# Performance work log

Hardware: AMD Instinct MI355X
Metric: run time of the kernel (lower is better)

Reference implementation:

```python
import jax, jax.numpy as jnp
import numpy as np

M0, S0 = 0.0, 2.0       # normal prior mean / std on mu, beta
SHAPE, SCALE = 2.0, 1.0  # gamma prior on softplus(phi)


def _softplus(x):
    return jnp.logaddexp(x, 0.0)


def _log_negbinomial(y, mu, phi):
    # NB parameterized by mean mu and dispersion phi (var = mu + phi*mu^2)
    r = 1.0 / phi
    return (jax.lax.lgamma(y + r) - jax.lax.lgamma(r) - jax.lax.lgamma(y + 1.0)
            + r * jnp.log(r / (r + mu)) + y * jnp.log(mu / (r + mu)))


def _log_normal(x, m, s):
    return -0.5 * jnp.log(2.0 * jnp.pi * s * s) - (x - m) ** 2 / (2.0 * s * s)


def _log_gamma(x, shape, scale):
    return ((shape - 1.0) * jnp.log(x) - x / scale
            - jax.lax.lgamma(jnp.asarray(shape, x.dtype)) - shape * jnp.log(scale))


def setup_inputs() -> dict:
    key = jax.random.key(0)
    k1, k2, k3, k4, k5 = jax.random.split(key, 5)
    N, P, G = 1024, 4, 20000
    X = jax.random.normal(k1, (N, P), dtype=jnp.float32)
    Y = jax.random.randint(k2, (N, G), 0, 500).astype(jnp.float32)
    mu = jax.random.normal(k3, (G,), dtype=jnp.float32)
    beta = jax.random.normal(k4, (P * G,), dtype=jnp.float32)
    phi = jax.random.normal(k5, (G,), dtype=jnp.float32)
    return {"X": X, "Y": Y, "mu": mu, "beta": beta, "phi": phi}


def reference(X, Y, mu, beta, phi):
    N, P = X.shape
    G = Y.shape[1]
    beta_ = beta.reshape(P, G)
    log_unnorm = mu + X @ beta_                                   # [N, G]
    norm = jax.scipy.special.logsumexp(log_unnorm, axis=1, keepdims=True)
    pi = jnp.exp(log_unnorm - norm)                               # softmax over genes
    s = jnp.sum(Y, axis=1, keepdims=True)                         # [N, 1] library sizes
    phi_sp = _softplus(phi)                                       # [G]
    log_lik = jnp.sum(_log_negbinomial(Y, s * pi, phi_sp))
    log_prior = (jnp.sum(_log_normal(mu, M0, S0))
                 + jnp.sum(_log_normal(beta, M0, S0))
                 + jnp.sum(_log_gamma(phi_sp, SHAPE, SCALE)))
    return (log_lik + log_prior).reshape(1)
```

## Files before the change

### kernel.cpp

```cpp
#include <hip/hip_runtime.h>
#include <math.h>


#define FG4   5000
#define FCH4  250
#define FNCH  20
#define FNSL  64
#define FNBLK 1280

__device__ __forceinline__ float fast_rcp(float x) {
    return __builtin_amdgcn_rcpf(x);
}

__device__ __forceinline__ float lgamma_pos(float x) {
    float lp = 0.0f;
    if (x < 8.0f) {
        float p = x;
        x += 1.0f;
        while (x < 8.0f) { p *= x; x += 1.0f; }
        lp = __logf(p);
    }
    float inv  = fast_rcp(x);
    float inv2 = inv * inv;
    float ser = inv * (0.08333333333f + inv2 * (-0.002777777778f + inv2 * 7.936507937e-4f));
    return (x - 0.5f) * __logf(x) - x + 0.9189385332f + ser - lp;
}

__device__ __forceinline__ float stirling_lg(float x) {
    float inv  = fast_rcp(x);
    float inv2 = inv * inv;
    float ser  = inv * (0.08333333333f - 0.002777777778f * inv2);
    return (x - 0.5f) * __logf(x) - x + 0.9189385332f + ser;
}

__device__ __forceinline__ float softplus_f(float x) {
    return fmaxf(x, 0.0f) + log1pf(__expf(-fabsf(x)));
}

__device__ __forceinline__ float wave_reduce(float v) {
#pragma unroll
    for (int off = 32; off; off >>= 1) v += __shfl_down(v, off, 64);
    return v;
}

__global__ __launch_bounds__(256) void setup_kernel(
        const float* __restrict__ mu, const float* __restrict__ beta,
        const float* __restrict__ phi, double* __restrict__ acc,
        float* __restrict__ rg, float* __restrict__ cgw, int P, int G) {
    int g = blockIdx.x * 256 + threadIdx.x;
    float v = 0.0f;
    if (g < G) {
        const float cn = -1.6120857137646180f;
        float m = mu[g];
        v = cn - m * m * 0.125f;
        for (int p = 0; p < P; ++p) {
            float b = beta[(size_t)p * G + g];
            v += cn - b * b * 0.125f;
        }
        float sp = softplus_f(phi[g]);
        v += __logf(sp) - sp;
        float r = 1.0f / sp;
        rg[g]  = r;
        cgw[g] = r * __logf(r) - lgamma_pos(r);
    }
    v = wave_reduce(v);
    __shared__ float red[4];
    int lane = threadIdx.x & 63, wid = threadIdx.x >> 6;
    if (lane == 0) red[wid] = v;
    __syncthreads();
    if (threadIdx.x == 0)
        atomicAdd(acc, (double)((red[0] + red[1]) + (red[2] + red[3])));
}

__global__ __launch_bounds__(256, 4) void pre_fast(
        const float* __restrict__ X, const float* __restrict__ Y,
        const float* __restrict__ mu, const float* __restrict__ beta,
        float* __restrict__ syw, float* __restrict__ sew) {
    __shared__ float Xs[64];
    __shared__ float syp[4][16], sep[4][16];

    const int tid  = threadIdx.x;
    const int lane = tid & 63, wid = tid >> 6;
    const int c    = blockIdx.x % FNCH;
    const int s    = blockIdx.x / FNCH;
    const int n0   = s * 16;
    const bool active = (tid < FCH4);
    const int gi4  = c * FCH4 + (active ? tid : FCH4 - 1);

    const float4* __restrict__ Yp = (const float4*)Y + (size_t)n0 * FG4 + gi4;
    float4 ya[16];
#pragma unroll
    for (int j = 0; j < 16; ++j) ya[j] = Yp[(size_t)j * FG4];

    if (tid < 64) Xs[tid] = X[(size_t)n0 * 4 + tid];
    const float4* __restrict__ B4 = (const float4*)beta;
    float4 bb[4], mug;
#pragma unroll
    for (int p = 0; p < 4; ++p) bb[p] = B4[(size_t)p * FG4 + gi4];
    mug = ((const float4*)mu)[gi4];
    __syncthreads();

#pragma unroll
    for (int i0 = 0; i0 < 16; i0 += 4) {
        float sy[4], se[4];
#pragma unroll
        for (int j = 0; j < 4; ++j) {
            const int i = i0 + j;
            float4 y = ya[i];
            float4 lu = mug;
#pragma unroll
            for (int p = 0; p < 4; ++p) {
                float xp = Xs[i * 4 + p];
                lu.x = fmaf(xp, bb[p].x, lu.x);
                lu.y = fmaf(xp, bb[p].y, lu.y);
                lu.z = fmaf(xp, bb[p].z, lu.z);
                lu.w = fmaf(xp, bb[p].w, lu.w);
            }
            float e = (__expf(lu.x) + __expf(lu.y)) + (__expf(lu.z) + __expf(lu.w));
            se[j] = active ? e : 0.0f;
            sy[j] = active ? ((y.x + y.y) + (y.z + y.w)) : 0.0f;
        }
#pragma unroll
        for (int off = 32; off; off >>= 1) {
#pragma unroll
            for (int j = 0; j < 4; ++j) {
                sy[j] += __shfl_down(sy[j], off, 64);
                se[j] += __shfl_down(se[j], off, 64);
            }
        }
        if (lane == 0) {
#pragma unroll
            for (int j = 0; j < 4; ++j) {
                syp[wid][i0 + j] = sy[j];
                sep[wid][i0 + j] = se[j];
            }
        }
    }
    __syncthreads();
    if (tid < 16) {
        float a = (syp[0][tid] + syp[1][tid]) + (syp[2][tid] + syp[3][tid]);
        float b = (sep[0][tid] + sep[1][tid]) + (sep[2][tid] + sep[3][tid]);
        atomicAdd(&syw[n0 + tid], a);
        atomicAdd(&sew[n0 + tid], b);
    }
}

__global__ __launch_bounds__(256, 4) void nb_fast(
        const float* __restrict__ X, const float* __restrict__ Y,
        const float* __restrict__ mu, const float* __restrict__ beta,
        const float* __restrict__ rg, const float* __restrict__ cgw,
        const float* __restrict__ syw, const float* __restrict__ sew,
        double* __restrict__ acc) {
    __shared__ float lgY[512];
    __shared__ float Xs[64];
    __shared__ float dcs[16];
    __shared__ float red[4];

    const int tid  = threadIdx.x;
    const int lane = tid & 63, wid = tid >> 6;
    const int c    = blockIdx.x % FNCH;
    const int s    = blockIdx.x / FNCH;
    const int n0   = s * 16;
    const bool active = (tid < FCH4);
    const int gi4  = c * FCH4 + (active ? tid : FCH4 - 1);

    const float4* __restrict__ Yp = (const float4*)Y + (size_t)n0 * FG4 + gi4;
    float4 ya[8];
#pragma unroll
    for (int j = 0; j < 8; ++j) ya[j] = Yp[(size_t)j * FG4];

    for (int i = tid; i < 500; i += 256) lgY[i] = lgamma_pos((float)(i + 1));
    if (tid < 64) Xs[tid] = X[(size_t)n0 * 4 + tid];
    if (tid < 16) dcs[tid] = __logf(syw[n0 + tid]) - __logf(sew[n0 + tid]);

    const float4* __restrict__ B4 = (const float4*)beta;
    float4 bb[4], mug, r4, cg4;
#pragma unroll
    for (int p = 0; p < 4; ++p) bb[p] = B4[(size_t)p * FG4 + gi4];
    mug = ((const float4*)mu)[gi4];
    r4  = ((const float4*)rg)[gi4];
    cg4 = ((const float4*)cgw)[gi4];
    __syncthreads();

    float t0 = 0.0f, t1 = 0.0f, t2 = 0.0f, t3 = 0.0f;
    auto elem = [&](int i, float4 y) {
        float dcn = dcs[i];
        float4 lu = mug;
#pragma unroll
        for (int p = 0; p < 4; ++p) {
            float xp = Xs[i * 4 + p];
            lu.x = fmaf(xp, bb[p].x, lu.x);
            lu.y = fmaf(xp, bb[p].y, lu.y);
            lu.z = fmaf(xp, bb[p].z, lu.z);
            lu.w = fmaf(xp, bb[p].w, lu.w);
        }
        float lm, m, yr;
        lm = dcn + lu.x; m = __expf(lm); yr = y.x + r4.x;
        t0 += stirling_lg(yr) - lgY[__float2int_rz(y.x)]
            + fmaf(y.x, lm, -yr * __logf(r4.x + m)) + cg4.x;
        lm = dcn + lu.y; m = __expf(lm); yr = y.y + r4.y;
        t1 += stirling_lg(yr) - lgY[__float2int_rz(y.y)]
            + fmaf(y.y, lm, -yr * __logf(r4.y + m)) + cg4.y;
        lm = dcn + lu.z; m = __expf(lm); yr = y.z + r4.z;
        t2 += stirling_lg(yr) - lgY[__float2int_rz(y.z)]
            + fmaf(y.z, lm, -yr * __logf(r4.z + m)) + cg4.z;
        lm = dcn + lu.w; m = __expf(lm); yr = y.w + r4.w;
        t3 += stirling_lg(yr) - lgY[__float2int_rz(y.w)]
            + fmaf(y.w, lm, -yr * __logf(r4.w + m)) + cg4.w;
    };

    float4 yb[8];
#pragma unroll
    for (int j = 0; j < 8; ++j) yb[j] = Yp[(size_t)(8 + j) * FG4];
#pragma unroll
    for (int i = 0; i < 8; ++i) elem(i, ya[i]);
#pragma unroll
    for (int i = 0; i < 8; ++i) elem(8 + i, yb[i]);

    float accl = active ? ((t0 + t1) + (t2 + t3)) : 0.0f;
    accl = wave_reduce(accl);
    if (lane == 0) red[wid] = accl;
    __syncthreads();
    if (tid == 0)
        atomicAdd(acc, (double)((red[0] + red[1]) + (red[2] + red[3])));
}

__global__ void finalize_kernel(const double* __restrict__ acc, float* __restrict__ out) {
    out[0] = (float)acc[0];
}

__global__ void row_stats_generic(
        const float* __restrict__ X, const float* __restrict__ Y,
        const float* __restrict__ mu, const float* __restrict__ beta,
        float* __restrict__ syw, float* __restrict__ sew, int N, int P, int G) {
    const int n = blockIdx.x;
    const int tid = threadIdx.x;
    float sy = 0.0f, se = 0.0f;
    for (int g = tid; g < G; g += 256) {
        sy += Y[(size_t)n * G + g];
        float lu = mu[g];
        for (int p = 0; p < P; ++p) lu += X[(size_t)n * P + p] * beta[(size_t)p * G + g];
        se += __expf(lu);
    }
    sy = wave_reduce(sy);
    se = wave_reduce(se);
    __shared__ float r1[4], r2[4];
    int lane = tid & 63, wid = tid >> 6;
    if (lane == 0) { r1[wid] = sy; r2[wid] = se; }
    __syncthreads();
    if (tid == 0) {
        syw[n] = (r1[0] + r1[1]) + (r1[2] + r1[3]);
        sew[n] = (r2[0] + r2[1]) + (r2[2] + r2[3]);
    }
}

__global__ void nb_generic(
        const float* __restrict__ X, const float* __restrict__ Y,
        const float* __restrict__ mu, const float* __restrict__ beta,
        const float* __restrict__ rg, const float* __restrict__ cgw,
        const float* __restrict__ syw, const float* __restrict__ sew,
        double* __restrict__ acc, int N, int P, int G) {
    const int n = blockIdx.x;
    const int tid = threadIdx.x;
    float dcn = __logf(syw[n]) - __logf(sew[n]);
    float accl = 0.0f;
    for (int g = tid; g < G; g += 256) {
        float y = Y[(size_t)n * G + g];
        float lu = mu[g];
        for (int p = 0; p < P; ++p) lu += X[(size_t)n * P + p] * beta[(size_t)p * G + g];
        float lm = dcn + lu;
        float r = rg[g];
        float m = __expf(lm);
        accl += stirling_lg(y + r) - lgamma_pos(y + 1.0f)
                + fmaf(y, lm, -(y + r) * __logf(r + m)) + cgw[g];
    }
    accl = wave_reduce(accl);
    __shared__ float red[4];
    int lane = tid & 63, wid = tid >> 6;
    if (lane == 0) red[wid] = accl;
    __syncthreads();
    if (tid == 0)
        atomicAdd(acc, (double)((red[0] + red[1]) + (red[2] + red[3])));
}

extern "C" void kernel_launch(void* const* d_in, const int* in_sizes, int n_in,
                              void* d_out, int out_size, void* d_ws, size_t ws_size,
                              hipStream_t stream) {
    const float* X    = (const float*)d_in[0];
    const float* Y    = (const float*)d_in[1];
    const float* mu   = (const float*)d_in[2];
    const float* beta = (const float*)d_in[3];
    const float* phi  = (const float*)d_in[4];
    float* out = (float*)d_out;

    const int G = in_sizes[2];
    const int N = in_sizes[1] / G;
    const int P = in_sizes[0] / N;

    char* ws = (char*)d_ws;
    double* acc = (double*)ws;
    float*  syw = (float*)(ws + 256);
    float*  sew = (float*)(ws + 4608);
    float*  rgw = (float*)(ws + 8960);
    float*  cgw = (float*)(ws + 8960 + (size_t)4 * G);

    hipMemsetAsync(d_ws, 0, 8960, stream);

    const bool fast_ok = (N == 1024 && G == 20000 && P == 4);
    int gblocks = (G + 255) / 256;

    if (fast_ok) {
        pre_fast<<<FNBLK, 256, 0, stream>>>(X, Y, mu, beta, syw, sew);
        setup_kernel<<<gblocks, 256, 0, stream>>>(mu, beta, phi, acc, rgw, cgw, P, G);
        nb_fast<<<FNBLK, 256, 0, stream>>>(X, Y, mu, beta, rgw, cgw, syw, sew, acc);
    } else {
        setup_kernel<<<gblocks, 256, 0, stream>>>(mu, beta, phi, acc, rgw, cgw, P, G);
        row_stats_generic<<<N, 256, 0, stream>>>(X, Y, mu, beta, syw, sew, N, P, G);
        nb_generic<<<N, 256, 0, stream>>>(X, Y, mu, beta, rgw, cgw, syw, sew,
                                          acc, N, P, G);
    }
    finalize_kernel<<<1, 1, 0, stream>>>(acc, out);
}
```

Measured before the change: 167.3 us.

## Fuse setup and finalize into pre/nb kernels, trim Stirling series

Moves the prior and per-gene rg/cgw computation into the first slice of pre_fast blocks, removing the separate setup_kernel launch. The final float conversion now happens in the last nb_fast block, found through an atomic completion counter, which replaces the single-thread finalize launch. The Stirling lgamma series drops its second-order term, saving a few instructions per element at some accuracy cost for small y+r. The intent is to cut two kernel launches and their gaps, in exchange for extra work in the s==0 blocks and a fence and atomic per block.

```diff
diff --git a/kernel.cpp b/kernel.cpp
--- a/kernel.cpp
+++ b/kernel.cpp
@@ -5,7 +5,6 @@
 #define FG4   5000
 #define FCH4  250
 #define FNCH  20
-#define FNSL  64
 #define FNBLK 1280
 
 __device__ __forceinline__ float fast_rcp(float x) {
@@ -27,10 +26,8 @@
 }
 
 __device__ __forceinline__ float stirling_lg(float x) {
-    float inv  = fast_rcp(x);
-    float inv2 = inv * inv;
-    float ser  = inv * (0.08333333333f - 0.002777777778f * inv2);
-    return (x - 0.5f) * __logf(x) - x + 0.9189385332f + ser;
+    float inv = fast_rcp(x);
+    return fmaf(x - 0.5f, __logf(x), 0.08333333333f * inv) - x + 0.9189385332f;
 }
 
 __device__ __forceinline__ float softplus_f(float x) {
@@ -43,41 +40,16 @@
     return v;
 }
 
-__global__ __launch_bounds__(256) void setup_kernel(
-        const float* __restrict__ mu, const float* __restrict__ beta,
-        const float* __restrict__ phi, double* __restrict__ acc,
-        float* __restrict__ rg, float* __restrict__ cgw, int P, int G) {
-    int g = blockIdx.x * 256 + threadIdx.x;
-    float v = 0.0f;
-    if (g < G) {
-        const float cn = -1.6120857137646180f;
-        float m = mu[g];
-        v = cn - m * m * 0.125f;
-        for (int p = 0; p < P; ++p) {
-            float b = beta[(size_t)p * G + g];
-            v += cn - b * b * 0.125f;
-        }
-        float sp = softplus_f(phi[g]);
-        v += __logf(sp) - sp;
-        float r = 1.0f / sp;
-        rg[g]  = r;
-        cgw[g] = r * __logf(r) - lgamma_pos(r);
-    }
-    v = wave_reduce(v);
-    __shared__ float red[4];
-    int lane = threadIdx.x & 63, wid = threadIdx.x >> 6;
-    if (lane == 0) red[wid] = v;
-    __syncthreads();
-    if (threadIdx.x == 0)
-        atomicAdd(acc, (double)((red[0] + red[1]) + (red[2] + red[3])));
-}
-
 __global__ __launch_bounds__(256, 4) void pre_fast(
         const float* __restrict__ X, const float* __restrict__ Y,
         const float* __restrict__ mu, const float* __restrict__ beta,
-        float* __restrict__ syw, float* __restrict__ sew) {
+        const float* __restrict__ phi,
+        float* __restrict__ syw, float* __restrict__ sew,
+        float* __restrict__ rgw, float* __restrict__ cgw,
+        double* __restrict__ acc) {
     __shared__ float Xs[64];
     __shared__ float syp[4][16], sep[4][16];
+    __shared__ float red[4];
 
     const int tid  = threadIdx.x;
     const int lane = tid & 63, wid = tid >> 6;
@@ -98,7 +70,43 @@
 #pragma unroll
     for (int p = 0; p < 4; ++p) bb[p] = B4[(size_t)p * FG4 + gi4];
     mug = ((const float4*)mu)[gi4];
-    __syncthreads();
+
+    float priorv = 0.0f;
+    if (s == 0) {
+        const float cn = -1.6120857137646180f;
+        float4 ph = ((const float4*)phi)[gi4];
+        float4 r4p, cg4p;
+        priorv += cn - mug.x * mug.x * 0.125f;
+        priorv += cn - mug.y * mug.y * 0.125f;
+        priorv += cn - mug.z * mug.z * 0.125f;
+        priorv += cn - mug.w * mug.w * 0.125f;
+#pragma unroll
+        for (int p = 0; p < 4; ++p) {
+            priorv += cn - bb[p].x * bb[p].x * 0.125f;
+            priorv += cn - bb[p].y * bb[p].y * 0.125f;
+            priorv += cn - bb[p].z * bb[p].z * 0.125f;
+            priorv += cn - bb[p].w * bb[p].w * 0.125f;
+        }
+        float sp;
+        sp = softplus_f(ph.x); priorv += __logf(sp) - sp; r4p.x = fast_rcp(sp);
+        cg4p.x = r4p.x * __logf(r4p.x) - lgamma_pos(r4p.x);
+        sp = softplus_f(ph.y); priorv += __logf(sp) - sp; r4p.y = fast_rcp(sp);
+        cg4p.y = r4p.y * __logf(r4p.y) - lgamma_pos(r4p.y);
+        sp = softplus_f(ph.z); priorv += __logf(sp) - sp; r4p.z = fast_rcp(sp);
+        cg4p.z = r4p.z * __logf(r4p.z) - lgamma_pos(r4p.z);
+        sp = softplus_f(ph.w); priorv += __logf(sp) - sp; r4p.w = fast_rcp(sp);
+        cg4p.w = r4p.w * __logf(r4p.w) - lgamma_pos(r4p.w);
+        if (active) {
+            ((float4*)rgw)[gi4] = r4p;
+            ((float4*)cgw)[gi4] = cg4p;
+        }
+        if (!active) priorv = 0.0f;
+        priorv = wave_reduce(priorv);
+        if (lane == 0) red[wid] = priorv;
+    }
+    __syncthreads();
+    if (s == 0 && tid == 0)
+        atomicAdd(acc, (double)((red[0] + red[1]) + (red[2] + red[3])));
 
 #pragma unroll
     for (int i0 = 0; i0 < 16; i0 += 4) {
@@ -150,7 +158,8 @@
         const float* __restrict__ mu, const float* __restrict__ beta,
         const float* __restrict__ rg, const float* __restrict__ cgw,
         const float* __restrict__ syw, const float* __restrict__ sew,
-        double* __restrict__ acc) {
+        double* __restrict__ acc, float* __restrict__ out,
+        unsigned int* __restrict__ counter) {
     __shared__ float lgY[512];
     __shared__ float Xs[64];
     __shared__ float dcs[16];
@@ -221,12 +230,44 @@
     accl = wave_reduce(accl);
     if (lane == 0) red[wid] = accl;
     __syncthreads();
-    if (tid == 0)
+    if (tid == 0) {
         atomicAdd(acc, (double)((red[0] + red[1]) + (red[2] + red[3])));
-}
-
-__global__ void finalize_kernel(const double* __restrict__ acc, float* __restrict__ out) {
-    out[0] = (float)acc[0];
+        __threadfence();
+        unsigned int old = atomicAdd(counter, 1u);
+        if (old == (unsigned int)(FNBLK - 1)) {
+            double v = atomicAdd(acc, 0.0);
+            out[0] = (float)v;
+        }
+    }
+}
+
+__global__ __launch_bounds__(256) void setup_kernel(
+        const float* __restrict__ mu, const float* __restrict__ beta,
+        const float* __restrict__ phi, double* __restrict__ acc,
+        float* __restrict__ rg, float* __restrict__ cgw, int P, int G) {
+    int g = blockIdx.x * 256 + threadIdx.x;
+    float v = 0.0f;
+    if (g < G) {
+        const float cn = -1.6120857137646180f;
+        float m = mu[g];
+        v = cn - m * m * 0.125f;
+        for (int p = 0; p < P; ++p) {
+            float b = beta[(size_t)p * G + g];
+            v += cn - b * b * 0.125f;
+        }
+        float sp = softplus_f(phi[g]);
+        v += __logf(sp) - sp;
+        float r = 1.0f / sp;
+        rg[g]  = r;
+        cgw[g] = r * __logf(r) - lgamma_pos(r);
+    }
+    v = wave_reduce(v);
+    __shared__ float red[4];
+    int lane = threadIdx.x & 63, wid = threadIdx.x >> 6;
+    if (lane == 0) red[wid] = v;
+    __syncthreads();
+    if (threadIdx.x == 0)
+        atomicAdd(acc, (double)((red[0] + red[1]) + (red[2] + red[3])));
 }
 
 __global__ void row_stats_generic(
@@ -283,6 +324,10 @@
         atomicAdd(acc, (double)((red[0] + red[1]) + (red[2] + red[3])));
 }
 
+__global__ void finalize_kernel(const double* __restrict__ acc, float* __restrict__ out) {
+    out[0] = (float)acc[0];
+}
+
 extern "C" void kernel_launch(void* const* d_in, const int* in_sizes, int n_in,
                               void* d_out, int out_size, void* d_ws, size_t ws_size,
                               hipStream_t stream) {
@@ -298,26 +343,28 @@
     const int P = in_sizes[0] / N;
 
     char* ws = (char*)d_ws;
-    double* acc = (double*)ws;
-    float*  syw = (float*)(ws + 256);
-    float*  sew = (float*)(ws + 4608);
-    float*  rgw = (float*)(ws + 8960);
-    float*  cgw = (float*)(ws + 8960 + (size_t)4 * G);
+    double*       acc     = (double*)ws;
+    unsigned int* counter = (unsigned int*)(ws + 64);
+    float*        syw     = (float*)(ws + 256);
+    float*        sew     = (float*)(ws + 4608);
+    float*        rgw     = (float*)(ws + 8960);
+    float*        cgw     = (float*)(ws + 8960 + (size_t)4 * G);
 
     hipMemsetAsync(d_ws, 0, 8960, stream);
 
     const bool fast_ok = (N == 1024 && G == 20000 && P == 4);
-    int gblocks = (G + 255) / 256;
 
     if (fast_ok) {
-        pre_fast<<<FNBLK, 256, 0, stream>>>(X, Y, mu, beta, syw, sew);
-        setup_kernel<<<gblocks, 256, 0, stream>>>(mu, beta, phi, acc, rgw, cgw, P, G);
-        nb_fast<<<FNBLK, 256, 0, stream>>>(X, Y, mu, beta, rgw, cgw, syw, sew, acc);
+        pre_fast<<<FNBLK, 256, 0, stream>>>(X, Y, mu, beta, phi,
+                                            syw, sew, rgw, cgw, acc);
+        nb_fast<<<FNBLK, 256, 0, stream>>>(X, Y, mu, beta, rgw, cgw,
+                                           syw, sew, acc, out, counter);
     } else {
+        int gblocks = (G + 255) / 256;
         setup_kernel<<<gblocks, 256, 0, stream>>>(mu, beta, phi, acc, rgw, cgw, P, G);
         row_stats_generic<<<N, 256, 0, stream>>>(X, Y, mu, beta, syw, sew, N, P, G);
         nb_generic<<<N, 256, 0, stream>>>(X, Y, mu, beta, rgw, cgw, syw, sew,
                                           acc, N, P, G);
-    }
-    finalize_kernel<<<1, 1, 0, stream>>>(acc, out);
-}
+        finalize_kernel<<<1, 1, 0, stream>>>(acc, out);
+    }
+}
```

New measurement: 182.5 us. 1.09x slower.
